# Kernel optimization log

Measured on AMD Instinct MI355X. Metric: run time of the kernel, lower is better.

Reference implementation:

```python
import jax, jax.numpy as jnp
import numpy as np

N, E, D, H, L = 50000, 800000, 64, 4, 2
DH = D // H


def layer_norm(h, g, b, eps=1e-5):
    mu = h.mean(-1, keepdims=True)
    var = ((h - mu) ** 2).mean(-1, keepdims=True)
    return (h - mu) / jnp.sqrt(var + eps) * g + b


def setup_inputs() -> dict:
    key = jax.random.key(0)
    ks = jax.random.split(key, 16)
    s = 1.0 / np.sqrt(D)
    inp = {
        "x": jax.random.normal(ks[0], (N, D), jnp.float32),
        "edge_attr": jax.random.normal(ks[1], (E, D), jnp.float32),
        "edge_index": jax.random.randint(ks[2], (2, E), 0, N, jnp.int64),
        "WQ": jax.random.normal(ks[3], (L, D, D), jnp.float32) * s,
        "WK": jax.random.normal(ks[4], (L, D, D), jnp.float32) * s,
        "WE": jax.random.normal(ks[5], (L, D, D), jnp.float32) * s,
        "WV": jax.random.normal(ks[6], (L, D, D), jnp.float32) * s,
        "WO": jax.random.normal(ks[7], (L, D, D), jnp.float32) * s,
        "bO": jnp.zeros((L, D), jnp.float32),
        "ln1_g": jnp.ones((L, D), jnp.float32),
        "ln1_b": jnp.zeros((L, D), jnp.float32),
        "W1": jax.random.normal(ks[8], (L, D, 2 * D), jnp.float32) * s,
        "b1": jnp.zeros((L, 2 * D), jnp.float32),
        "W2": jax.random.normal(ks[9], (L, 2 * D, D), jnp.float32) * (1.0 / np.sqrt(2 * D)),
        "b2": jnp.zeros((L, D), jnp.float32),
        "ln2_g": jnp.ones((L, D), jnp.float32),
        "ln2_b": jnp.zeros((L, D), jnp.float32),
    }
    return inp


def exphormer_layer(h, edge_attr, src, dst, p):
    (wq, wk, we, wv, wo, bo, g1, be1, w1, b1, w2, b2, g2, be2) = p
    n = h.shape[0]
    Qh = (h @ wq).reshape(n, H, DH)
    Kh = (h @ wk).reshape(n, H, DH)
    Vh = (h @ wv).reshape(n, H, DH)
    Eh = (edge_attr @ we).reshape(-1, H, DH)
    # per-edge score: sum over head_dim of K[src]*Q[dst]*E / sqrt(DH)
    s = jnp.sum(Kh[src] * Qh[dst] * Eh, axis=-1, keepdims=True) / np.sqrt(DH)
    score = jnp.exp(jnp.clip(s, -5.0, 5.0))  # [E, H, 1]
    msg = Vh[src] * score                     # [E, H, DH]
    wV = jax.ops.segment_sum(msg, dst, num_segments=n)    # [N, H, DH]
    Z = jax.ops.segment_sum(score, dst, num_segments=n)   # [N, H, 1]
    h_attn = (wV / (Z + 1e-6)).reshape(n, D)
    h1 = layer_norm(h + (h_attn @ wo + bo), g1, be1)
    ffn = jax.nn.relu(h1 @ w1 + b1) @ w2 + b2
    return layer_norm(h1 + ffn, g2, be2)


def reference(x, edge_attr, edge_index, WQ, WK, WE, WV, WO, bO, ln1_g, ln1_b,
              W1, b1, W2, b2, ln2_g, ln2_b):
    src = edge_index[0]
    dst = edge_index[1]
    h = x
    for l in range(L):
        p = (WQ[l], WK[l], WE[l], WV[l], WO[l], bO[l], ln1_g[l], ln1_b[l],
             W1[l], b1[l], W2[l], b2[l], ln2_g[l], ln2_b[l])
        h = exphormer_layer(h, edge_attr, src, dst, p)
    return h
```

## Files before the change

kernel.cpp:

```cpp
#include <hip/hip_runtime.h>

#define NN 50000
#define NE 800000
#define D  64
#define NL 2

typedef __bf16 bf16x8 __attribute__((ext_vector_type(8)));
typedef float  floatx4 __attribute__((ext_vector_type(4)));

static __device__ __forceinline__ float bf2f(unsigned short u) {
    return __uint_as_float(((unsigned)u) << 16);
}
static __device__ __forceinline__ unsigned short f2bf(float x) {
    unsigned u = __float_as_uint(x);
    u += 0x7fff + ((u >> 16) & 1);
    return (unsigned short)(u >> 16);
}


__global__ void k_deg(const int* __restrict__ ei, int* __restrict__ deg) {
    int e = blockIdx.x * 256 + threadIdx.x;
    if (e < NE) atomicAdd(&deg[ei[NE + e]], 1);
}

__global__ void k_scan(const int* __restrict__ deg, int* __restrict__ row_off,
                       int* __restrict__ cursor) {
    __shared__ int buf[1024];
    __shared__ int carry_s;
    if (threadIdx.x == 0) carry_s = 0;
    __syncthreads();
    for (int base = 0; base < NN; base += 1024) {
        int i = base + (int)threadIdx.x;
        int v = (i < NN) ? deg[i] : 0;
        buf[threadIdx.x] = v;
        __syncthreads();
        for (int offt = 1; offt < 1024; offt <<= 1) {
            int t = (threadIdx.x >= (unsigned)offt) ? buf[threadIdx.x - offt] : 0;
            __syncthreads();
            buf[threadIdx.x] += t;
            __syncthreads();
        }
        int inc = buf[threadIdx.x] + carry_s;
        if (i < NN) {
            row_off[i + 1] = inc;
            cursor[i] = inc - v;
            if (i == 0) row_off[0] = 0;
        }
        __syncthreads();
        if (threadIdx.x == 1023) carry_s = inc;
        __syncthreads();
    }
}

__global__ void k_scatter(const int* __restrict__ ei, int* __restrict__ cursor,
                          int* __restrict__ csr_src, int* __restrict__ eperm) {
    int e = blockIdx.x * 256 + threadIdx.x;
    if (e < NE) {
        int dst = ei[NE + e];
        int pos = atomicAdd(&cursor[dst], 1);
        csr_src[pos] = ei[e];
        eperm[e] = pos;
    }
}

__global__ __launch_bounds__(256) void k_prep(
        const float* __restrict__ WQ, const float* __restrict__ WK,
        const float* __restrict__ WV, const float* __restrict__ WE,
        const float* __restrict__ WO, const float* __restrict__ W1,
        const float* __restrict__ W2,
        unsigned short* __restrict__ wqT, unsigned short* __restrict__ wkT,
        unsigned short* __restrict__ wvT, unsigned short* __restrict__ weT,
        unsigned short* __restrict__ woT, unsigned short* __restrict__ w1T,
        unsigned short* __restrict__ w2T) {
    int idx = blockIdx.x * 256 + threadIdx.x;
    if (idx >= 2 * 36864) return;
    int l = idx / 36864;
    int r = idx % 36864;
    if (r < 20480) {
        int which = r >> 12, rr = r & 4095;
        int m = rr >> 6, k = rr & 63;
        const float* src = (which == 0 ? WQ : which == 1 ? WK : which == 2 ? WV :
                            which == 3 ? WE : WO);
        unsigned short* dst = (which == 0 ? wqT : which == 1 ? wkT : which == 2 ? wvT :
                               which == 3 ? weT : woT);
        dst[l * 4096 + rr] = f2bf(src[l * 4096 + k * 64 + m]);
    } else if (r < 28672) {
        int r2 = r - 20480;
        int m = r2 >> 6, k = r2 & 63;
        w1T[l * 8192 + r2] = f2bf(W1[l * 8192 + k * 128 + m]);
    } else {
        int r3 = r - 28672;
        int m = r3 >> 7, k = r3 & 127;
        w2T[l * 8192 + r3] = f2bf(W2[l * 8192 + k * 64 + m]);
    }
}


__global__ __launch_bounds__(256) void k_qkv_mfma(const float* __restrict__ h,
        const unsigned short* __restrict__ wqT, const unsigned short* __restrict__ wkT,
        const unsigned short* __restrict__ wvT,
        float* __restrict__ Qh, unsigned short* __restrict__ Kb,
        unsigned short* __restrict__ Vb) {
    __shared__ unsigned short st[4][16 * 72];
    const int lane = threadIdx.x & 63;
    const int w    = threadIdx.x >> 6;
    const int ml   = lane & 15;
    const int quad = lane >> 4;

    bf16x8 aq[2][4], ak[2][4], av[2][4];
#pragma unroll
    for (int kt = 0; kt < 2; kt++)
#pragma unroll
        for (int mt = 0; mt < 4; mt++) {
            int o = (mt*16 + ml)*64 + kt*32 + quad*8;
            aq[kt][mt] = *(const bf16x8*)&wqT[o];
            ak[kt][mt] = *(const bf16x8*)&wkT[o];
            av[kt][mt] = *(const bf16x8*)&wvT[o];
        }

    const int wave = blockIdx.x * 4 + w;
    const int nw   = gridDim.x * 4;
    for (int tile = wave; tile < NN / 16; tile += nw) {
        const int e0 = tile * 16;
        const float4* ar = (const float4*)(h + (size_t)(e0 + ml) * D);
        bf16x8 b[2];
#pragma unroll
        for (int kt = 0; kt < 2; kt++) {
            float4 f0 = ar[kt*8 + quad*2 + 0];
            float4 f1 = ar[kt*8 + quad*2 + 1];
            b[kt][0] = (__bf16)f0.x; b[kt][1] = (__bf16)f0.y;
            b[kt][2] = (__bf16)f0.z; b[kt][3] = (__bf16)f0.w;
            b[kt][4] = (__bf16)f1.x; b[kt][5] = (__bf16)f1.y;
            b[kt][6] = (__bf16)f1.z; b[kt][7] = (__bf16)f1.w;
        }
        floatx4 accq[4] = {}, acck[4] = {}, accv[4] = {};
#pragma unroll
        for (int kt = 0; kt < 2; kt++)
#pragma unroll
            for (int mt = 0; mt < 4; mt++) {
                accq[mt] = __builtin_amdgcn_mfma_f32_16x16x32_bf16(aq[kt][mt], b[kt], accq[mt], 0, 0, 0);
                acck[mt] = __builtin_amdgcn_mfma_f32_16x16x32_bf16(ak[kt][mt], b[kt], acck[mt], 0, 0, 0);
                accv[mt] = __builtin_amdgcn_mfma_f32_16x16x32_bf16(av[kt][mt], b[kt], accv[mt], 0, 0, 0);
            }
#pragma unroll
        for (int mt = 0; mt < 4; mt++)
            *(float4*)(Qh + (size_t)(e0 + ml) * D + mt*16 + quad*4) =
                make_float4(accq[mt][0], accq[mt][1], accq[mt][2], accq[mt][3]);
        const int el = lane >> 2, c = lane & 3;
#pragma unroll
        for (int mt = 0; mt < 4; mt++)
            *(ushort4*)&st[w][ml*72 + mt*16 + quad*4] =
                make_ushort4(f2bf(acck[mt][0]), f2bf(acck[mt][1]),
                             f2bf(acck[mt][2]), f2bf(acck[mt][3]));
        {
            uint4 r0 = *(const uint4*)&st[w][el*72 + c*16 + 0];
            uint4 r1 = *(const uint4*)&st[w][el*72 + c*16 + 8];
            uint4* gp = (uint4*)(Kb + (size_t)(e0 + el) * D + c*16);
            gp[0] = r0; gp[1] = r1;
        }
#pragma unroll
        for (int mt = 0; mt < 4; mt++)
            *(ushort4*)&st[w][ml*72 + mt*16 + quad*4] =
                make_ushort4(f2bf(accv[mt][0]), f2bf(accv[mt][1]),
                             f2bf(accv[mt][2]), f2bf(accv[mt][3]));
        {
            uint4 r0 = *(const uint4*)&st[w][el*72 + c*16 + 0];
            uint4 r1 = *(const uint4*)&st[w][el*72 + c*16 + 8];
            uint4* gp = (uint4*)(Vb + (size_t)(e0 + el) * D + c*16);
            gp[0] = r0; gp[1] = r1;
        }
    }
}

__global__ __launch_bounds__(256) void k_eh_mfma(const float* __restrict__ ea,
        const unsigned short* __restrict__ weT, const int* __restrict__ eperm,
        unsigned short* __restrict__ Eh) {
    __shared__ unsigned short st[4][16 * 72];
    const int lane = threadIdx.x & 63;
    const int w    = threadIdx.x >> 6;
    const int ml   = lane & 15;
    const int quad = lane >> 4;

    bf16x8 afr[2][2][4];
#pragma unroll
    for (int l = 0; l < 2; l++)
#pragma unroll
        for (int kt = 0; kt < 2; kt++)
#pragma unroll
            for (int mt = 0; mt < 4; mt++)
                afr[l][kt][mt] = *(const bf16x8*)&weT[l*4096 + (mt*16 + ml)*64 + kt*32 + quad*8];

    const int wave = blockIdx.x * 4 + w;
    const int nw   = gridDim.x * 4;
    const int el = lane >> 2, c = lane & 3;
    for (int tile = wave; tile < NE / 16; tile += nw) {
        const int e0 = tile * 16;
        const float4* ar = (const float4*)(ea + (size_t)(e0 + ml) * D);
        bf16x8 b[2];
#pragma unroll
        for (int kt = 0; kt < 2; kt++) {
            float4 f0 = ar[kt*8 + quad*2 + 0];
            float4 f1 = ar[kt*8 + quad*2 + 1];
            b[kt][0] = (__bf16)f0.x; b[kt][1] = (__bf16)f0.y;
            b[kt][2] = (__bf16)f0.z; b[kt][3] = (__bf16)f0.w;
            b[kt][4] = (__bf16)f1.x; b[kt][5] = (__bf16)f1.y;
            b[kt][6] = (__bf16)f1.z; b[kt][7] = (__bf16)f1.w;
        }
        int pos = eperm[e0 + el];
#pragma unroll
        for (int l = 0; l < 2; l++) {
            floatx4 acc[4] = {};
#pragma unroll
            for (int kt = 0; kt < 2; kt++)
#pragma unroll
                for (int mt = 0; mt < 4; mt++)
                    acc[mt] = __builtin_amdgcn_mfma_f32_16x16x32_bf16(afr[l][kt][mt], b[kt], acc[mt], 0, 0, 0);
#pragma unroll
            for (int mt = 0; mt < 4; mt++)
                *(ushort4*)&st[w][ml*72 + mt*16 + quad*4] =
                    make_ushort4(f2bf(acc[mt][0]), f2bf(acc[mt][1]),
                                 f2bf(acc[mt][2]), f2bf(acc[mt][3]));
            uint4 r0 = *(const uint4*)&st[w][el*72 + c*16 + 0];
            uint4 r1 = *(const uint4*)&st[w][el*72 + c*16 + 8];
            uint4* gp = (uint4*)(Eh + (size_t)l * NE * D + (size_t)pos * D + c*16);
            gp[0] = r0;
            gp[1] = r1;
        }
    }
}

__global__ __launch_bounds__(256) void k_agg(const float* __restrict__ Qh,
        const unsigned short* __restrict__ Kb, const unsigned short* __restrict__ Vb,
        const unsigned short* __restrict__ Eh,
        const int* __restrict__ row_off, const int* __restrict__ csr_src,
        float* __restrict__ h_attn) {
    const int node = blockIdx.x * 4 + (threadIdx.x >> 6);
    if (node >= NN) return;
    const int lane  = threadIdx.x & 63;
    const int eslot = lane >> 4;
    const int ml    = lane & 15;
    const int beg = row_off[node], end = row_off[node + 1];
    const float4 q = ((const float4*)(Qh + (size_t)node * D))[ml];
    float4 acc = make_float4(0.f, 0.f, 0.f, 0.f);
    float z = 0.f;

    int i0 = beg + eslot;
    while (i0 < end) {
        int i1 = i0 + 4;
        bool a1 = i1 < end;
        int s0 = csr_src[i0];
        int p1 = a1 ? i1 : i0;
        int s1 = a1 ? csr_src[p1] : s0;
        ushort4 kb0 = *(const ushort4*)(Kb + (size_t)s0 * D + ml * 4);
        ushort4 eb0 = *(const ushort4*)(Eh + (size_t)i0 * D + ml * 4);
        ushort4 vb0 = *(const ushort4*)(Vb + (size_t)s0 * D + ml * 4);
        ushort4 kb1 = *(const ushort4*)(Kb + (size_t)s1 * D + ml * 4);
        ushort4 eb1 = *(const ushort4*)(Eh + (size_t)p1 * D + ml * 4);
        ushort4 vb1 = *(const ushort4*)(Vb + (size_t)s1 * D + ml * 4);

        float part0 = bf2f(kb0.x) * q.x * bf2f(eb0.x) + bf2f(kb0.y) * q.y * bf2f(eb0.y)
                    + bf2f(kb0.z) * q.z * bf2f(eb0.z) + bf2f(kb0.w) * q.w * bf2f(eb0.w);
        float part1 = bf2f(kb1.x) * q.x * bf2f(eb1.x) + bf2f(kb1.y) * q.y * bf2f(eb1.y)
                    + bf2f(kb1.z) * q.z * bf2f(eb1.z) + bf2f(kb1.w) * q.w * bf2f(eb1.w);
        part0 += __shfl_xor(part0, 1, 64);
        part0 += __shfl_xor(part0, 2, 64);
        part1 += __shfl_xor(part1, 1, 64);
        part1 += __shfl_xor(part1, 2, 64);
        float sc0 = __expf(fminf(5.f, fmaxf(-5.f, part0 * 0.25f)));
        float sc1 = a1 ? __expf(fminf(5.f, fmaxf(-5.f, part1 * 0.25f))) : 0.f;

        acc.x += sc0 * bf2f(vb0.x) + sc1 * bf2f(vb1.x);
        acc.y += sc0 * bf2f(vb0.y) + sc1 * bf2f(vb1.y);
        acc.z += sc0 * bf2f(vb0.z) + sc1 * bf2f(vb1.z);
        acc.w += sc0 * bf2f(vb0.w) + sc1 * bf2f(vb1.w);
        z += sc0 + sc1;
        i0 += 8;
    }
#pragma unroll
    for (int m = 16; m <= 32; m <<= 1) {
        acc.x += __shfl_xor(acc.x, m, 64);
        acc.y += __shfl_xor(acc.y, m, 64);
        acc.z += __shfl_xor(acc.z, m, 64);
        acc.w += __shfl_xor(acc.w, m, 64);
        z     += __shfl_xor(z, m, 64);
    }
    if (eslot == 0) {
        float inv = 1.f / (z + 1e-6f);
        ((float4*)(h_attn + (size_t)node * D))[ml] =
            make_float4(acc.x * inv, acc.y * inv, acc.z * inv, acc.w * inv);
    }
}

__global__ __launch_bounds__(512) void k_post_mfma(const float* __restrict__ h_in,
        const float* __restrict__ h_attn,
        const unsigned short* __restrict__ woT_g,
        const unsigned short* __restrict__ w1T_g,
        const unsigned short* __restrict__ w2T_g,
        const float* __restrict__ bo,
        const float* __restrict__ g1, const float* __restrict__ be1,
        const float* __restrict__ b1, const float* __restrict__ b2,
        const float* __restrict__ g2, const float* __restrict__ be2,
        float* __restrict__ h_out) {
    __shared__ unsigned short woT_s[64 * 72];
    __shared__ unsigned short w1T_s[128 * 72];
    __shared__ unsigned short w2T_s[64 * 136];
    __shared__ unsigned short stg[8][16 * 136];

    const int t = threadIdx.x;
    {
        const uint4* s0 = (const uint4*)woT_g;
        { int i = t; if (i < 512) { int row = i >> 3, c = i & 7;
              *(uint4*)&woT_s[row*72 + c*8] = s0[i]; } }
        const uint4* s1 = (const uint4*)w1T_g;
        for (int i = t; i < 1024; i += 512) {
            int row = i >> 3, c = i & 7;
            *(uint4*)&w1T_s[row*72 + c*8] = s1[i];
        }
        const uint4* s2 = (const uint4*)w2T_g;
        for (int i = t; i < 1024; i += 512) {
            int row = i >> 4, c = i & 15;
            *(uint4*)&w2T_s[row*136 + c*8] = s2[i];
        }
    }
    __syncthreads();

    const int w = t >> 6, lane = t & 63;
    const int ml = lane & 15, quad = lane >> 4;
    const int tile = blockIdx.x * 8 + w;
    if (tile >= NN / 16) return;
    const int e0 = tile * 16;
    unsigned short* st = stg[w];

    const float4* ap = (const float4*)(h_attn + (size_t)(e0 + ml) * D);
    floatx4 acc1[4] = {};
#pragma unroll
    for (int kt = 0; kt < 2; kt++) {
        float4 f0 = ap[kt*8 + quad*2 + 0];
        float4 f1 = ap[kt*8 + quad*2 + 1];
        bf16x8 b;
        b[0] = (__bf16)f0.x; b[1] = (__bf16)f0.y; b[2] = (__bf16)f0.z; b[3] = (__bf16)f0.w;
        b[4] = (__bf16)f1.x; b[5] = (__bf16)f1.y; b[6] = (__bf16)f1.z; b[7] = (__bf16)f1.w;
#pragma unroll
        for (int mt = 0; mt < 4; mt++) {
            bf16x8 a = *(const bf16x8*)&woT_s[(mt*16 + ml)*72 + kt*32 + quad*8];
            acc1[mt] = __builtin_amdgcn_mfma_f32_16x16x32_bf16(a, b, acc1[mt], 0, 0, 0);
        }
    }
    const float4* hp  = (const float4*)(h_in + (size_t)(e0 + ml) * D);
    const float4* bo4 = (const float4*)bo;
    floatx4 tt[4];
#pragma unroll
    for (int mt = 0; mt < 4; mt++) {
        float4 hh = hp[mt*4 + quad];
        float4 bb = bo4[mt*4 + quad];
        tt[mt][0] = acc1[mt][0] + hh.x + bb.x;
        tt[mt][1] = acc1[mt][1] + hh.y + bb.y;
        tt[mt][2] = acc1[mt][2] + hh.z + bb.z;
        tt[mt][3] = acc1[mt][3] + hh.w + bb.w;
    }
    float s = 0.f;
#pragma unroll
    for (int mt = 0; mt < 4; mt++) s += tt[mt][0] + tt[mt][1] + tt[mt][2] + tt[mt][3];
    s += __shfl_xor(s, 16, 64); s += __shfl_xor(s, 32, 64);
    float mu = s * (1.f / 64.f);
    float v = 0.f;
#pragma unroll
    for (int mt = 0; mt < 4; mt++)
#pragma unroll
        for (int r = 0; r < 4; r++) { float c = tt[mt][r] - mu; v += c * c; }
    v += __shfl_xor(v, 16, 64); v += __shfl_xor(v, 32, 64);
    float rstd = rsqrtf(v * (1.f / 64.f) + 1e-5f);
    const float4* g1v  = (const float4*)g1;
    const float4* be1v = (const float4*)be1;
    floatx4 h1[4];
#pragma unroll
    for (int mt = 0; mt < 4; mt++) {
        float4 gg = g1v[mt*4 + quad];
        float4 bb = be1v[mt*4 + quad];
        h1[mt][0] = (tt[mt][0] - mu) * rstd * gg.x + bb.x;
        h1[mt][1] = (tt[mt][1] - mu) * rstd * gg.y + bb.y;
        h1[mt][2] = (tt[mt][2] - mu) * rstd * gg.z + bb.z;
        h1[mt][3] = (tt[mt][3] - mu) * rstd * gg.w + bb.w;
        *(ushort4*)&st[ml*136 + mt*16 + quad*4] =
            make_ushort4(f2bf(h1[mt][0]), f2bf(h1[mt][1]), f2bf(h1[mt][2]), f2bf(h1[mt][3]));
    }

    bf16x8 bh[2];
#pragma unroll
    for (int kt = 0; kt < 2; kt++)
        bh[kt] = *(const bf16x8*)&st[ml*136 + kt*32 + quad*8];
    floatx4 acc2[8] = {};
#pragma unroll
    for (int kt = 0; kt < 2; kt++)
#pragma unroll
        for (int mt = 0; mt < 8; mt++) {
            bf16x8 a = *(const bf16x8*)&w1T_s[(mt*16 + ml)*72 + kt*32 + quad*8];
            acc2[mt] = __builtin_amdgcn_mfma_f32_16x16x32_bf16(a, bh[kt], acc2[mt], 0, 0, 0);
        }
    const float4* b1v = (const float4*)b1;
#pragma unroll
    for (int mt = 0; mt < 8; mt++) {
        float4 bb = b1v[mt*4 + quad];
        float y0 = fmaxf(acc2[mt][0] + bb.x, 0.f);
        float y1 = fmaxf(acc2[mt][1] + bb.y, 0.f);
        float y2 = fmaxf(acc2[mt][2] + bb.z, 0.f);
        float y3 = fmaxf(acc2[mt][3] + bb.w, 0.f);
        *(ushort4*)&st[ml*136 + mt*16 + quad*4] =
            make_ushort4(f2bf(y0), f2bf(y1), f2bf(y2), f2bf(y3));
    }

    floatx4 acc3[4] = {};
#pragma unroll
    for (int kt = 0; kt < 4; kt++) {
        bf16x8 b = *(const bf16x8*)&st[ml*136 + kt*32 + quad*8];
#pragma unroll
        for (int mt = 0; mt < 4; mt++) {
            bf16x8 a = *(const bf16x8*)&w2T_s[(mt*16 + ml)*136 + kt*32 + quad*8];
            acc3[mt] = __builtin_amdgcn_mfma_f32_16x16x32_bf16(a, b, acc3[mt], 0, 0, 0);
        }
    }
    const float4* b2v = (const float4*)b2;
#pragma unroll
    for (int mt = 0; mt < 4; mt++) {
        float4 bb = b2v[mt*4 + quad];
        tt[mt][0] = acc3[mt][0] + bb.x + h1[mt][0];
        tt[mt][1] = acc3[mt][1] + bb.y + h1[mt][1];
        tt[mt][2] = acc3[mt][2] + bb.z + h1[mt][2];
        tt[mt][3] = acc3[mt][3] + bb.w + h1[mt][3];
    }
    s = 0.f;
#pragma unroll
    for (int mt = 0; mt < 4; mt++) s += tt[mt][0] + tt[mt][1] + tt[mt][2] + tt[mt][3];
    s += __shfl_xor(s, 16, 64); s += __shfl_xor(s, 32, 64);
    mu = s * (1.f / 64.f);
    v = 0.f;
#pragma unroll
    for (int mt = 0; mt < 4; mt++)
#pragma unroll
        for (int r = 0; r < 4; r++) { float c = tt[mt][r] - mu; v += c * c; }
    v += __shfl_xor(v, 16, 64); v += __shfl_xor(v, 32, 64);
    rstd = rsqrtf(v * (1.f / 64.f) + 1e-5f);
    const float4* g2v  = (const float4*)g2;
    const float4* be2v = (const float4*)be2;
    float4* outp = (float4*)(h_out + (size_t)(e0 + ml) * D);
#pragma unroll
    for (int mt = 0; mt < 4; mt++) {
        float4 gg = g2v[mt*4 + quad];
        float4 bb = be2v[mt*4 + quad];
        float4 o;
        o.x = (tt[mt][0] - mu) * rstd * gg.x + bb.x;
        o.y = (tt[mt][1] - mu) * rstd * gg.y + bb.y;
        o.z = (tt[mt][2] - mu) * rstd * gg.z + bb.z;
        o.w = (tt[mt][3] - mu) * rstd * gg.w + bb.w;
        outp[mt*4 + quad] = o;
    }
}


extern "C" void kernel_launch(void* const* d_in, const int* in_sizes, int n_in,
                              void* d_out, int out_size, void* d_ws, size_t ws_size,
                              hipStream_t stream) {
    const float* x   = (const float*)d_in[0];
    const float* ea  = (const float*)d_in[1];
    const int*   ei  = (const int*)d_in[2];
    const float* WQ  = (const float*)d_in[3];
    const float* WK  = (const float*)d_in[4];
    const float* WE  = (const float*)d_in[5];
    const float* WV  = (const float*)d_in[6];
    const float* WO  = (const float*)d_in[7];
    const float* bO  = (const float*)d_in[8];
    const float* g1  = (const float*)d_in[9];
    const float* be1 = (const float*)d_in[10];
    const float* W1  = (const float*)d_in[11];
    const float* b1  = (const float*)d_in[12];
    const float* W2  = (const float*)d_in[13];
    const float* b2  = (const float*)d_in[14];
    const float* g2  = (const float*)d_in[15];
    const float* be2 = (const float*)d_in[16];
    float* out = (float*)d_out;

    char* wsb = (char*)d_ws;
    size_t off = 0;
    auto alloc = [&](size_t bytes) {
        void* p = wsb + off;
        off += (bytes + 255) & ~(size_t)255;
        return p;
    };
    float* Qh            = (float*)alloc((size_t)NN * D * 4);
    unsigned short* Kb   = (unsigned short*)alloc((size_t)NN * D * 2);
    unsigned short* Vb   = (unsigned short*)alloc((size_t)NN * D * 2);
    float* hbuf          = (float*)alloc((size_t)NN * D * 4);
    float* hattn         = (float*)alloc((size_t)NN * D * 4);
    unsigned short* Eh   = (unsigned short*)alloc((size_t)NL * NE * D * 2);
    int* row_off         = (int*)alloc((size_t)(NN + 1) * 4);
    int* cursor          = (int*)alloc((size_t)NN * 4);
    int* deg             = (int*)alloc((size_t)NN * 4);
    int* csr_src         = (int*)alloc((size_t)NE * 4);
    int* eperm           = (int*)alloc((size_t)NE * 4);
    unsigned short* wqT  = (unsigned short*)alloc((size_t)2 * 4096 * 2);
    unsigned short* wkT  = (unsigned short*)alloc((size_t)2 * 4096 * 2);
    unsigned short* wvT  = (unsigned short*)alloc((size_t)2 * 4096 * 2);
    unsigned short* weT  = (unsigned short*)alloc((size_t)2 * 4096 * 2);
    unsigned short* woT  = (unsigned short*)alloc((size_t)2 * 4096 * 2);
    unsigned short* w1T  = (unsigned short*)alloc((size_t)2 * 8192 * 2);
    unsigned short* w2T  = (unsigned short*)alloc((size_t)2 * 8192 * 2);

    hipMemsetAsync(deg, 0, (size_t)NN * 4, stream);
    k_deg<<<(NE + 255) / 256, 256, 0, stream>>>(ei, deg);
    k_scan<<<1, 1024, 0, stream>>>(deg, row_off, cursor);
    k_scatter<<<(NE + 255) / 256, 256, 0, stream>>>(ei, cursor, csr_src, eperm);
    k_prep<<<(2 * 36864 + 255) / 256, 256, 0, stream>>>(WQ, WK, WV, WE, WO, W1, W2,
            wqT, wkT, wvT, weT, woT, w1T, w2T);
    k_eh_mfma<<<1024, 256, 0, stream>>>(ea, weT, eperm, Eh);

    for (int l = 0; l < NL; l++) {
        const float* hcur = (l == 0) ? x : hbuf;
        float* hnxt = (l == NL - 1) ? out : hbuf;
        k_qkv_mfma<<<782, 256, 0, stream>>>(hcur, wqT + l * 4096, wkT + l * 4096,
                                            wvT + l * 4096, Qh, Kb, Vb);
        k_agg<<<(NN + 3) / 4, 256, 0, stream>>>(Qh, Kb, Vb, Eh + (size_t)l * NE * D,
                                                row_off, csr_src, hattn);
        k_post_mfma<<<(NN / 16 + 7) / 8, 512, 0, stream>>>(hcur, hattn,
                woT + l * 4096, w1T + l * 8192, w2T + l * 8192,
                bO + l * 64, g1 + l * 64, be1 + l * 64,
                b1 + l * 128, b2 + l * 64,
                g2 + l * 64, be2 + l * 64, hnxt);
    }
}
```

Baseline: 710.5 us.

## Parallelize CSR offset scan and batch edge-source loads in aggregation

The single-block serial prefix scan over node degrees becomes a three-kernel reduce, scan and add-back across 196 blocks, so it no longer runs on one workgroup. In the aggregation kernel, each wavefront now loads up to 64 CSR source indices with one coalesced read and hands them out by shuffle. It then processes four edges per lane slot per step, which puts more independent gathers in flight. The cost is two extra kernel launches and more registers in the aggregation loop.

```diff
diff --git a/kernel.cpp b/kernel.cpp
--- a/kernel.cpp
+++ b/kernel.cpp
@@ -4,6 +4,7 @@
 #define NE 800000
 #define D  64
 #define NL 2
+#define NB 196
 
 typedef __bf16 bf16x8 __attribute__((ext_vector_type(8)));
 typedef float  floatx4 __attribute__((ext_vector_type(4)));
@@ -23,32 +24,54 @@
     if (e < NE) atomicAdd(&deg[ei[NE + e]], 1);
 }
 
-__global__ void k_scan(const int* __restrict__ deg, int* __restrict__ row_off,
-                       int* __restrict__ cursor) {
-    __shared__ int buf[1024];
-    __shared__ int carry_s;
-    if (threadIdx.x == 0) carry_s = 0;
+__global__ __launch_bounds__(256) void k_scan1(const int* __restrict__ deg,
+                                               int* __restrict__ psum) {
+    __shared__ int red[4];
+    int i = blockIdx.x * 256 + threadIdx.x;
+    int v = (i < NN) ? deg[i] : 0;
+#pragma unroll
+    for (int m = 1; m < 64; m <<= 1) v += __shfl_xor(v, m, 64);
+    if ((threadIdx.x & 63) == 0) red[threadIdx.x >> 6] = v;
     __syncthreads();
-    for (int base = 0; base < NN; base += 1024) {
-        int i = base + (int)threadIdx.x;
-        int v = (i < NN) ? deg[i] : 0;
-        buf[threadIdx.x] = v;
+    if (threadIdx.x == 0) psum[blockIdx.x] = red[0] + red[1] + red[2] + red[3];
+}
+
+__global__ void k_scan2(int* __restrict__ psum) {
+    __shared__ int buf[256];
+    int t = threadIdx.x;
+    int v = (t < NB) ? psum[t] : 0;
+    buf[t] = v;
+    __syncthreads();
+    for (int o = 1; o < 256; o <<= 1) {
+        int x = (t >= o) ? buf[t - o] : 0;
         __syncthreads();
-        for (int offt = 1; offt < 1024; offt <<= 1) {
-            int t = (threadIdx.x >= (unsigned)offt) ? buf[threadIdx.x - offt] : 0;
-            __syncthreads();
-            buf[threadIdx.x] += t;
-            __syncthreads();
-        }
-        int inc = buf[threadIdx.x] + carry_s;
-        if (i < NN) {
-            row_off[i + 1] = inc;
-            cursor[i] = inc - v;
-            if (i == 0) row_off[0] = 0;
-        }
+        buf[t] += x;
         __syncthreads();
-        if (threadIdx.x == 1023) carry_s = inc;
+    }
+    if (t < NB) psum[t] = buf[t] - v;
+}
+
+__global__ __launch_bounds__(256) void k_scan3(const int* __restrict__ deg,
+                                               const int* __restrict__ psum,
+                                               int* __restrict__ row_off,
+                                               int* __restrict__ cursor) {
+    __shared__ int buf[256];
+    int t = threadIdx.x;
+    int i = blockIdx.x * 256 + t;
+    int v = (i < NN) ? deg[i] : 0;
+    buf[t] = v;
+    __syncthreads();
+    for (int o = 1; o < 256; o <<= 1) {
+        int x = (t >= o) ? buf[t - o] : 0;
         __syncthreads();
+        buf[t] += x;
+        __syncthreads();
+    }
+    if (i < NN) {
+        int inc = buf[t] + psum[blockIdx.x];
+        row_off[i + 1] = inc;
+        cursor[i] = inc - v;
+        if (i == 0) row_off[0] = 0;
     }
 }
 
@@ -244,37 +267,45 @@
     float4 acc = make_float4(0.f, 0.f, 0.f, 0.f);
     float z = 0.f;
 
-    int i0 = beg + eslot;
-    while (i0 < end) {
-        int i1 = i0 + 4;
-        bool a1 = i1 < end;
-        int s0 = csr_src[i0];
-        int p1 = a1 ? i1 : i0;
-        int s1 = a1 ? csr_src[p1] : s0;
-        ushort4 kb0 = *(const ushort4*)(Kb + (size_t)s0 * D + ml * 4);
-        ushort4 eb0 = *(const ushort4*)(Eh + (size_t)i0 * D + ml * 4);
-        ushort4 vb0 = *(const ushort4*)(Vb + (size_t)s0 * D + ml * 4);
-        ushort4 kb1 = *(const ushort4*)(Kb + (size_t)s1 * D + ml * 4);
-        ushort4 eb1 = *(const ushort4*)(Eh + (size_t)p1 * D + ml * 4);
-        ushort4 vb1 = *(const ushort4*)(Vb + (size_t)s1 * D + ml * 4);
-
-        float part0 = bf2f(kb0.x) * q.x * bf2f(eb0.x) + bf2f(kb0.y) * q.y * bf2f(eb0.y)
-                    + bf2f(kb0.z) * q.z * bf2f(eb0.z) + bf2f(kb0.w) * q.w * bf2f(eb0.w);
-        float part1 = bf2f(kb1.x) * q.x * bf2f(eb1.x) + bf2f(kb1.y) * q.y * bf2f(eb1.y)
-                    + bf2f(kb1.z) * q.z * bf2f(eb1.z) + bf2f(kb1.w) * q.w * bf2f(eb1.w);
-        part0 += __shfl_xor(part0, 1, 64);
-        part0 += __shfl_xor(part0, 2, 64);
-        part1 += __shfl_xor(part1, 1, 64);
-        part1 += __shfl_xor(part1, 2, 64);
-        float sc0 = __expf(fminf(5.f, fmaxf(-5.f, part0 * 0.25f)));
-        float sc1 = a1 ? __expf(fminf(5.f, fmaxf(-5.f, part1 * 0.25f))) : 0.f;
-
-        acc.x += sc0 * bf2f(vb0.x) + sc1 * bf2f(vb1.x);
-        acc.y += sc0 * bf2f(vb0.y) + sc1 * bf2f(vb1.y);
-        acc.z += sc0 * bf2f(vb0.z) + sc1 * bf2f(vb1.z);
-        acc.w += sc0 * bf2f(vb0.w) + sc1 * bf2f(vb1.w);
-        z += sc0 + sc1;
-        i0 += 8;
+    for (int cbeg = beg; cbeg < end; cbeg += 64) {
+        const int cnt = min(64, end - cbeg);
+        int myidx = cbeg + lane;
+        int mysrc = (myidx < end) ? csr_src[myidx] : 0;
+
+        for (int base = 0; base < cnt; base += 16) {
+            int  jj[4];
+            int  s[4];
+            bool act[4];
+#pragma unroll
+            for (int u = 0; u < 4; u++) {
+                int j = base + eslot + 4 * u;
+                act[u] = j < cnt;
+                jj[u]  = act[u] ? j : 0;
+                s[u]   = __shfl(mysrc, jj[u], 64);
+            }
+            ushort4 kb[4], eb[4], vb[4];
+#pragma unroll
+            for (int u = 0; u < 4; u++) {
+                kb[u] = *(const ushort4*)(Kb + (size_t)s[u] * D + ml * 4);
+                eb[u] = *(const ushort4*)(Eh + (size_t)(cbeg + jj[u]) * D + ml * 4);
+                vb[u] = *(const ushort4*)(Vb + (size_t)s[u] * D + ml * 4);
+            }
+#pragma unroll
+            for (int u = 0; u < 4; u++) {
+                float part = bf2f(kb[u].x) * q.x * bf2f(eb[u].x)
+                           + bf2f(kb[u].y) * q.y * bf2f(eb[u].y)
+                           + bf2f(kb[u].z) * q.z * bf2f(eb[u].z)
+                           + bf2f(kb[u].w) * q.w * bf2f(eb[u].w);
+                part += __shfl_xor(part, 1, 64);
+                part += __shfl_xor(part, 2, 64);
+                float sc = act[u] ? __expf(fminf(5.f, fmaxf(-5.f, part * 0.25f))) : 0.f;
+                acc.x += sc * bf2f(vb[u].x);
+                acc.y += sc * bf2f(vb[u].y);
+                acc.z += sc * bf2f(vb[u].z);
+                acc.w += sc * bf2f(vb[u].w);
+                z += sc;
+            }
+        }
     }
 #pragma unroll
     for (int m = 16; m <= 32; m <<= 1) {
@@ -495,6 +526,7 @@
     int* row_off         = (int*)alloc((size_t)(NN + 1) * 4);
     int* cursor          = (int*)alloc((size_t)NN * 4);
     int* deg             = (int*)alloc((size_t)NN * 4);
+    int* psum            = (int*)alloc((size_t)256 * 4);
     int* csr_src         = (int*)alloc((size_t)NE * 4);
     int* eperm           = (int*)alloc((size_t)NE * 4);
     unsigned short* wqT  = (unsigned short*)alloc((size_t)2 * 4096 * 2);
@@ -507,7 +539,9 @@
 
     hipMemsetAsync(deg, 0, (size_t)NN * 4, stream);
     k_deg<<<(NE + 255) / 256, 256, 0, stream>>>(ei, deg);
-    k_scan<<<1, 1024, 0, stream>>>(deg, row_off, cursor);
+    k_scan1<<<NB, 256, 0, stream>>>(deg, psum);
+    k_scan2<<<1, 256, 0, stream>>>(psum);
+    k_scan3<<<NB, 256, 0, stream>>>(deg, psum, row_off, cursor);
     k_scatter<<<(NE + 255) / 256, 256, 0, stream>>>(ei, cursor, csr_src, eperm);
     k_prep<<<(2 * 36864 + 255) / 256, 256, 0, stream>>>(WQ, WK, WV, WE, WO, W1, W2,
             wqT, wkT, wvT, weT, woT, w1T, w2T);
```

Result: faster. 611.3 us (-14.0%).
